# Optimization experiments

Measured on AMD Instinct MI355X. Metric: run time of the kernel, lower is better.

The kernel has to match this reference:

```python
import jax, jax.numpy as jnp
import numpy as np

D_MODEL, D_LOW, NUM_BINS = 512, 64, 39
DIST_MIN, DIST_MAX = 2.0, 22.0
BIN_WIDTH = (DIST_MAX - DIST_MIN) / (NUM_BINS - 1)
LN_EPS = 1e-5


def setup_inputs() -> dict:
    key = jax.random.key(0)
    ks = jax.random.split(key, 10)
    B, N = 2, 768
    h_res = jax.random.normal(ks[0], (B, N, D_MODEL), dtype=jnp.float32)
    # scale coords so pairwise distances span the [2, 22] bin range
    x_true = jax.random.normal(ks[1], (B, N, 3), dtype=jnp.float32) * 5.0
    token_pad_mask = jnp.ones((B, N), dtype=jnp.float32)
    s = 1.0 / np.sqrt(D_MODEL)
    return {
        "h_res": h_res,
        "x_true": x_true,
        "token_pad_mask": token_pad_mask,
        "ln_w": jnp.ones((D_MODEL,), jnp.float32),
        "ln_b": jnp.zeros((D_MODEL,), jnp.float32),
        "wu_w": jax.random.normal(ks[2], (D_LOW, D_MODEL), jnp.float32) * s,
        "wu_b": jnp.zeros((D_LOW,), jnp.float32),
        "wv_w": jax.random.normal(ks[3], (D_LOW, D_MODEL), jnp.float32) * s,
        "wv_b": jnp.zeros((D_LOW,), jnp.float32),
        "wb_w": jax.random.normal(ks[4], (NUM_BINS, D_LOW), jnp.float32) * (1.0 / np.sqrt(D_LOW)),
        "wb_b": jnp.zeros((NUM_BINS,), jnp.float32),
    }


def _layernorm(x, w, b):
    mu = jnp.mean(x, axis=-1, keepdims=True)
    var = jnp.mean(jnp.square(x - mu), axis=-1, keepdims=True)
    return (x - mu) * jax.lax.rsqrt(var + LN_EPS) * w + b


def reference(h_res, x_true, token_pad_mask, ln_w, ln_b, wu_w, wu_b, wv_w, wv_b, wb_w, wb_b):
    B, N, _ = h_res.shape
    # pairwise distances -> target bins (trunc-to-int then clamp, as torch .long())
    diff = x_true[:, :, None, :] - x_true[:, None, :, :]          # [B,N,N,3]
    d_true = jnp.sqrt(jnp.sum(diff * diff, axis=-1))               # [B,N,N]
    target = jnp.clip(((d_true - DIST_MIN) / BIN_WIDTH).astype(jnp.int32), 0, NUM_BINS - 1)

    h = _layernorm(h_res, ln_w, ln_b)
    U = h @ wu_w.T + wu_b                                          # [B,N,d_low]
    V = h @ wv_w.T + wv_b                                          # [B,N,d_low]
    # logits[b,i,j,k] = sum_c U[b,i,c] V[b,j,c] Wb[k,c] + bb[k]
    logits = jnp.einsum("bic,bjc,kc->bijk", U, V, wb_w) + wb_b     # [B,N,N,K]
    logp = jax.nn.log_softmax(logits, axis=-1)
    ce = -jnp.take_along_axis(logp, target[..., None], axis=-1)[..., 0]  # [B,N,N]

    mask = (token_pad_mask[:, :, None] * token_pad_mask[:, None, :]) > 0  # [B,N,N] bool
    counts = jnp.sum(mask, axis=(1, 2))                            # [B]
    per_sample = jnp.sum(jnp.where(mask, ce, 0.0), axis=(1, 2)) / jnp.maximum(counts, 1)
    valid = counts > 0
    total_count = jnp.sum(valid)
    loss = jnp.sum(jnp.where(valid, per_sample, 0.0)) / jnp.maximum(total_count, 1)
    return loss
```

## Files before the change

kernel.cpp:

```cpp
#include <hip/hip_runtime.h>
#include <hip/hip_bf16.h>
#include <math.h>

#define D_MODEL 512
#define D_LOW   64
#define NBINS   39
#define LOG2E   1.4426950408889634f
#define LN2     0.6931471805599453f

typedef __attribute__((ext_vector_type(8))) short short8;
typedef __attribute__((ext_vector_type(4))) float floatx4;

__global__ __launch_bounds__(256) void prep_tbin_kernel(
    const float* __restrict__ ln_w, const float* __restrict__ ln_b,
    const float* __restrict__ wu_w, const float* __restrict__ wu_b,
    const float* __restrict__ wv_w, const float* __restrict__ wv_b,
    const float* __restrict__ x_true, const float* __restrict__ pmask,
    __hip_bfloat16* __restrict__ w2bf, float* __restrict__ w2sum,
    float* __restrict__ b2, signed char* __restrict__ tbg, int N) {
  const int tid = threadIdx.x;

  if ((int)blockIdx.x >= 128) {
    const int p = blockIdx.x - 128;
    const int b = (p >= N) ? 1 : 0;
    const int i = p - b * N;
    const int rowi = b * N + i;
    const float xi0 = x_true[rowi * 3 + 0];
    const float xi1 = x_true[rowi * 3 + 1];
    const float xi2 = x_true[rowi * 3 + 2];
    const float pmi = pmask[rowi];
    const float BW  = (22.0f - 2.0f) / 38.0f;
    signed char* tbp = tbg + (size_t)b * N * N + (size_t)i * N;
    for (int j = tid; j < N; j += 256) {
      const int rowj = b * N + j;
      const float dx = xi0 - x_true[rowj * 3 + 0];
      const float dy = xi1 - x_true[rowj * 3 + 1];
      const float dz = xi2 - x_true[rowj * 3 + 2];
      const float d  = sqrtf(dx * dx + dy * dy + dz * dz);
      int tb = (int)((d - 2.0f) / BW);
      tb = tb < 0 ? 0 : (tb > NBINS - 1 ? NBINS - 1 : tb);
      tbp[j] = (pmi * pmask[rowj] > 0.f) ? (signed char)tb : (signed char)-1;
    }
    return;
  }

  __shared__ float red[8];
  const int o = blockIdx.x;
  const bool isU = (o < 64);
  const float* wrow = isU ? (wu_w + o * D_MODEL) : (wv_w + (o - 64) * D_MODEL);
  const float scale = isU ? LOG2E : 1.0f;

  float s1 = 0.f, s2 = 0.f;
  #pragma unroll
  for (int cc = 0; cc < 2; ++cc) {
    const int c = tid + cc * 256;
    const float w  = wrow[c];
    const float w2 = w * ln_w[c] * scale;
    const __hip_bfloat16 hb = __float2bfloat16(w2);
    w2bf[o * D_MODEL + c] = hb;
    s1 += __bfloat162float(hb);
    s2 += w * ln_b[c];
  }
  #pragma unroll
  for (int off = 32; off; off >>= 1) {
    s1 += __shfl_xor(s1, off);
    s2 += __shfl_xor(s2, off);
  }
  const int wave = tid >> 6, lane = tid & 63;
  if (lane == 0) { red[wave] = s1; red[4 + wave] = s2; }
  __syncthreads();
  if (tid == 0) {
    w2sum[o] = red[0] + red[1] + red[2] + red[3];
    const float ss2 = red[4] + red[5] + red[6] + red[7];
    b2[o] = scale * ((isU ? wu_b[o] : wv_b[o - 64]) + ss2);
  }
}

__global__ __launch_bounds__(64) void lnproj_kernel(
    const float* __restrict__ h_res, const __hip_bfloat16* __restrict__ w2bf,
    const float* __restrict__ w2sum, const float* __restrict__ b2,
    float* __restrict__ U, __hip_bfloat16* __restrict__ Vbf, int N) {
  const int lane = threadIdx.x;
  const int q = lane >> 4, ln16 = lane & 15;
  const int rt = blockIdx.x >> 2, og = blockIdx.x & 3;
  const int row0 = rt * 16;
  const float* hp = h_res + (size_t)(row0 + ln16) * D_MODEL + q * 8;

  short8 abf[16];
  float sum = 0.f, ssq = 0.f;
  #pragma unroll
  for (int kc = 0; kc < 16; ++kc) {
    const floatx4 x0 = *reinterpret_cast<const floatx4*>(hp + kc * 32);
    const floatx4 x1 = *reinterpret_cast<const floatx4*>(hp + kc * 32 + 4);
    short8 a;
    #pragma unroll
    for (int e = 0; e < 4; ++e) {
      sum += x0[e]; ssq += x0[e] * x0[e];
      const __hip_bfloat16 hb = __float2bfloat16(x0[e]);
      a[e] = *reinterpret_cast<const short*>(&hb);
    }
    #pragma unroll
    for (int e = 0; e < 4; ++e) {
      sum += x1[e]; ssq += x1[e] * x1[e];
      const __hip_bfloat16 hb = __float2bfloat16(x1[e]);
      a[4 + e] = *reinterpret_cast<const short*>(&hb);
    }
    abf[kc] = a;
  }
  sum += __shfl_xor(sum, 16); sum += __shfl_xor(sum, 32);
  ssq += __shfl_xor(ssq, 16); ssq += __shfl_xor(ssq, 32);
  const float mu  = sum * (1.0f / (float)D_MODEL);
  const float var = ssq * (1.0f / (float)D_MODEL) - mu * mu;
  const float rs  = rsqrtf(var + 1e-5f);
  float mu_r[4], rs_r[4];
  #pragma unroll
  for (int r = 0; r < 4; ++r) {
    mu_r[r] = __shfl(mu, q * 4 + r);
    rs_r[r] = __shfl(rs, q * 4 + r);
  }

  const int obase = og * 32;
  const int out0 = obase + ln16;
  const int out1 = obase + 16 + ln16;
  const short* wp = reinterpret_cast<const short*>(w2bf);
  floatx4 acc0 = (floatx4){0.f, 0.f, 0.f, 0.f};
  floatx4 acc1 = (floatx4){0.f, 0.f, 0.f, 0.f};
  #pragma unroll
  for (int kc = 0; kc < 16; ++kc) {
    const short8 b0 = *reinterpret_cast<const short8*>(
        wp + (size_t)out0 * D_MODEL + kc * 32 + q * 8);
    const short8 b1 = *reinterpret_cast<const short8*>(
        wp + (size_t)out1 * D_MODEL + kc * 32 + q * 8);
    acc0 = __builtin_amdgcn_mfma_f32_16x16x32_bf16(abf[kc], b0, acc0, 0, 0, 0);
    acc1 = __builtin_amdgcn_mfma_f32_16x16x32_bf16(abf[kc], b1, acc1, 0, 0, 0);
  }

  #pragma unroll
  for (int nt = 0; nt < 2; ++nt) {
    const int out  = nt ? out1 : out0;
    const floatx4 a = nt ? acc1 : acc0;
    const float ws = w2sum[out];
    const float bb = b2[out];
    #pragma unroll
    for (int r = 0; r < 4; ++r) {
      const int rowg = row0 + q * 4 + r;
      const float val = rs_r[r] * a[r] - mu_r[r] * rs_r[r] * ws + bb;
      if (out < 64) {
        U[(size_t)rowg * D_LOW + out] = val;
      } else {
        Vbf[(size_t)rowg * D_LOW + (out - 64)] = __float2bfloat16(val);
      }
    }
  }
}

__global__ __launch_bounds__(256) void wprep_kernel(
    const float* __restrict__ U, const float* __restrict__ wb_w,
    short* __restrict__ wfragbuf, int BN) {
  __shared__ float wsh[NBINS * 65];
  const int tid = threadIdx.x;
  for (int e = tid; e < NBINS * D_LOW; e += 256) {
    const int n = e >> 6, c = e & 63;
    wsh[n * 65 + c] = wb_w[e];
  }
  __syncthreads();

  const int wave = tid >> 6, lane = tid & 63;
  const int q = lane >> 4, ln16 = lane & 15;
  const int rowi = blockIdx.x * 4 + wave;
  const float* Up = U + (size_t)rowi * D_LOW;

  float u[16];
  #pragma unroll
  for (int s = 0; s < 2; ++s)
    #pragma unroll
    for (int e = 0; e < 8; ++e) u[s * 8 + e] = Up[s * 32 + q * 8 + e];

  short* outp = wfragbuf + (size_t)rowi * 6 * 64 * 8;
  #pragma unroll
  for (int t = 0; t < 3; ++t) {
    const int n = t * 16 + ln16;
    #pragma unroll
    for (int s = 0; s < 2; ++s) {
      short8 f;
      #pragma unroll
      for (int e = 0; e < 8; ++e) {
        const float w = (n < NBINS) ? wsh[n * 65 + s * 32 + q * 8 + e] : 0.f;
        const float v = u[s * 8 + e] * w;
        const __hip_bfloat16 hb = __float2bfloat16(v);
        f[e] = *reinterpret_cast<const short*>(&hb);
      }
      *reinterpret_cast<short8*>(outp + ((size_t)(t * 2 + s) * 64 + lane) * 8) = f;
    }
  }
}

__global__ __launch_bounds__(256) void pair_mfma_kernel(
    const short* __restrict__ wfragbuf,
    const __hip_bfloat16* __restrict__ Vbf,
    const float* __restrict__ wb_b,
    const signed char* __restrict__ tbg,
    float* __restrict__ part, int N) {
  __shared__ float rbuf[8];
  const int i    = blockIdx.x;
  const int b    = blockIdx.y >> 1;
  const int half = blockIdx.y & 1;
  const int tid  = threadIdx.x;
  const int wave = tid >> 6, lane = tid & 63;
  const int q = lane >> 4, ln16 = lane & 15;
  const int rowi = b * N + i;

  short8 wfrag[3][2];
  {
    const short* wfp = wfragbuf + (size_t)rowi * 6 * 64 * 8;
    #pragma unroll
    for (int t = 0; t < 3; ++t)
      #pragma unroll
      for (int s = 0; s < 2; ++s)
        wfrag[t][s] = *reinterpret_cast<const short8*>(
            wfp + ((size_t)(t * 2 + s) * 64 + lane) * 8);
  }

  floatx4 bias_init[3];
  #pragma unroll
  for (int t = 0; t < 3; ++t)
    #pragma unroll
    for (int r = 0; r < 4; ++r) {
      const int bin = t * 16 + q * 4 + r;
      bias_init[t][r] = (bin < NBINS) ? LOG2E * wb_b[bin] : -INFINITY;
    }

  const short* Vp = reinterpret_cast<const short*>(Vbf) + (size_t)b * N * D_LOW;
  const signed char* tbp = tbg + (size_t)b * N * N + (size_t)i * N;
  const int jbase = half * 384 + wave * 96;
  const int q4 = q * 4;

  float ce_sum = 0.f, cnt_sum = 0.f;

  short8 v[2][2];
  int tbv[2];
  {
    #pragma unroll
    for (int tt = 0; tt < 2; ++tt) {
      const size_t jr = jbase + tt * 16 + ln16;
      v[tt][0] = *reinterpret_cast<const short8*>(Vp + jr * D_LOW + q * 8);
      v[tt][1] = *reinterpret_cast<const short8*>(Vp + jr * D_LOW + 32 + q * 8);
      tbv[tt]  = (int)tbp[jr];
    }
  }

  for (int g = 0; g < 3; ++g) {
    short8 vn[2][2];
    int tbn[2];
    if (g < 2) {
      const int jb = jbase + (g + 1) * 32;
      #pragma unroll
      for (int tt = 0; tt < 2; ++tt) {
        const size_t jr = jb + tt * 16 + ln16;
        vn[tt][0] = *reinterpret_cast<const short8*>(Vp + jr * D_LOW + q * 8);
        vn[tt][1] = *reinterpret_cast<const short8*>(Vp + jr * D_LOW + 32 + q * 8);
        tbn[tt]   = (int)tbp[jr];
      }
    }

    floatx4 f[2][3];
    #pragma unroll
    for (int tt = 0; tt < 2; ++tt)
      #pragma unroll
      for (int t = 0; t < 3; ++t) {
        floatx4 a = bias_init[t];
        a = __builtin_amdgcn_mfma_f32_16x16x32_bf16(wfrag[t][0], v[tt][0], a, 0, 0, 0);
        a = __builtin_amdgcn_mfma_f32_16x16x32_bf16(wfrag[t][1], v[tt][1], a, 0, 0, 0);
        f[tt][t] = a;
      }

    #pragma unroll
    for (int tt = 0; tt < 2; ++tt) {
      const int tb  = tbv[tt];
      const int tbq = tb - q4;
      float s0 = 0.f, s1 = 0.f, s2 = 0.f, s3 = 0.f, lt = 0.f;
      #pragma unroll
      for (int t = 0; t < 3; ++t) {
        const floatx4 fv = f[tt][t];
        s0 += __builtin_amdgcn_exp2f(fv[0]);
        s1 += __builtin_amdgcn_exp2f(fv[1]);
        s2 += __builtin_amdgcn_exp2f(fv[2]);
        s3 += __builtin_amdgcn_exp2f(fv[3]);
        lt += (tbq == t * 16 + 0) ? fv[0] : 0.f;
        lt += (tbq == t * 16 + 1) ? fv[1] : 0.f;
        lt += (tbq == t * 16 + 2) ? fv[2] : 0.f;
        lt += (tbq == t * 16 + 3) ? fv[3] : 0.f;
      }
      float ssum = (s0 + s1) + (s2 + s3);
      ssum += __shfl_xor(ssum, 16); ssum += __shfl_xor(ssum, 32);
      const float ok = (tb >= 0) ? 1.f : 0.f;
      ce_sum  += ok * LN2 * (__builtin_amdgcn_logf(ssum) - 4.0f * lt);
      cnt_sum += ok;
    }

    if (g < 2) {
      #pragma unroll
      for (int tt = 0; tt < 2; ++tt) {
        v[tt][0] = vn[tt][0]; v[tt][1] = vn[tt][1]; tbv[tt] = tbn[tt];
      }
    }
  }

  #pragma unroll
  for (int off = 32; off; off >>= 1) {
    ce_sum  += __shfl_xor(ce_sum, off);
    cnt_sum += __shfl_xor(cnt_sum, off);
  }
  if (lane == 0) { rbuf[wave] = ce_sum; rbuf[4 + wave] = cnt_sum; }
  __syncthreads();
  if (tid == 0) {
    const size_t slot = ((size_t)(b * 2 + half) * N + i) * 2;
    part[slot + 0] = rbuf[0] + rbuf[1] + rbuf[2] + rbuf[3];
    part[slot + 1] = rbuf[4] + rbuf[5] + rbuf[6] + rbuf[7];
  }
}

__global__ __launch_bounds__(256) void finalize_kernel(
    const float* __restrict__ part, float* __restrict__ out, int N, int B) {
  __shared__ float red[8];
  const int tid = threadIdx.x, wave = tid >> 6, lane = tid & 63;
  float loss = 0.f, vcount = 0.f;
  for (int b = 0; b < B; ++b) {
    float ce = 0.f, cnt = 0.f;
    for (int e = tid; e < 2 * N; e += 256) {
      const size_t base = ((size_t)b * 2 * N + e) * 2;
      ce  += part[base + 0];
      cnt += part[base + 1];
    }
    #pragma unroll
    for (int off = 32; off; off >>= 1) {
      ce  += __shfl_xor(ce, off);
      cnt += __shfl_xor(cnt, off);
    }
    if (lane == 0) { red[wave] = ce; red[4 + wave] = cnt; }
    __syncthreads();
    if (tid == 0) {
      const float s = red[0] + red[1] + red[2] + red[3];
      const float c = red[4] + red[5] + red[6] + red[7];
      if (c > 0.f) { loss += s / fmaxf(c, 1.f); vcount += 1.f; }
    }
    __syncthreads();
  }
  if (tid == 0) out[0] = (vcount > 0.f) ? loss / vcount : 0.f;
}

extern "C" void kernel_launch(void* const* d_in, const int* in_sizes, int n_in,
                              void* d_out, int out_size, void* d_ws, size_t ws_size,
                              hipStream_t stream) {
  const float* h_res  = (const float*)d_in[0];
  const float* x_true = (const float*)d_in[1];
  const float* pmask  = (const float*)d_in[2];
  const float* ln_w   = (const float*)d_in[3];
  const float* ln_b   = (const float*)d_in[4];
  const float* wu_w   = (const float*)d_in[5];
  const float* wu_b   = (const float*)d_in[6];
  const float* wv_w   = (const float*)d_in[7];
  const float* wv_b   = (const float*)d_in[8];
  const float* wb_w   = (const float*)d_in[9];
  const float* wb_b   = (const float*)d_in[10];

  const int B  = 2;
  const int N  = in_sizes[2] / B;
  const int BN = B * N;

  float* U = (float*)d_ws;
  __hip_bfloat16* Vbf = (__hip_bfloat16*)(U + (size_t)BN * D_LOW);
  float* part = (float*)(Vbf + (size_t)BN * D_LOW);
  signed char* tbg = (signed char*)(part + 4 * (size_t)BN);
  short* wfragbuf = (short*)(tbg + (size_t)B * N * N);
  __hip_bfloat16* w2bf = (__hip_bfloat16*)(wfragbuf + (size_t)BN * 6 * 64 * 8);
  float* w2sum = (float*)(w2bf + 128 * D_MODEL);
  float* b2    = w2sum + 128;

  prep_tbin_kernel<<<128 + BN, 256, 0, stream>>>(
      ln_w, ln_b, wu_w, wu_b, wv_w, wv_b, x_true, pmask,
      w2bf, w2sum, b2, tbg, N);
  lnproj_kernel<<<(BN / 16) * 4, 64, 0, stream>>>(h_res, w2bf, w2sum, b2,
                                                  U, Vbf, N);
  wprep_kernel<<<BN / 4, 256, 0, stream>>>(U, wb_w, wfragbuf, BN);
  pair_mfma_kernel<<<dim3(N, 2 * B), 256, 0, stream>>>(wfragbuf, Vbf, wb_b,
                                                       tbg, part, N);
  finalize_kernel<<<1, 256, 0, stream>>>(part, (float*)d_out, N, B);
}
```

Before: 118.5 us.

## Fuse target-bin computation into pair kernel and merge projection with wfrag prep

```diff
diff --git a/kernel.cpp b/kernel.cpp
--- a/kernel.cpp
+++ b/kernel.cpp
@@ -11,26 +11,179 @@
 typedef __attribute__((ext_vector_type(8))) short short8;
 typedef __attribute__((ext_vector_type(4))) float floatx4;
 
-__global__ __launch_bounds__(256) void prep_tbin_kernel(
+__global__ __launch_bounds__(256) void prep_kernel(
     const float* __restrict__ ln_w, const float* __restrict__ ln_b,
     const float* __restrict__ wu_w, const float* __restrict__ wu_b,
     const float* __restrict__ wv_w, const float* __restrict__ wv_b,
+    __hip_bfloat16* __restrict__ w2bf, float* __restrict__ w2sum,
+    float* __restrict__ b2) {
+  __shared__ float red[8];
+  const int tid = threadIdx.x;
+  const int o = blockIdx.x;
+  const bool isU = (o < 64);
+  const float* wrow = isU ? (wu_w + o * D_MODEL) : (wv_w + (o - 64) * D_MODEL);
+  const float scale = isU ? LOG2E : 1.0f;
+
+  float s1 = 0.f, s2 = 0.f;
+  #pragma unroll
+  for (int cc = 0; cc < 2; ++cc) {
+    const int c = tid + cc * 256;
+    const float w  = wrow[c];
+    const float w2 = w * ln_w[c] * scale;
+    const __hip_bfloat16 hb = __float2bfloat16(w2);
+    w2bf[o * D_MODEL + c] = hb;
+    s1 += __bfloat162float(hb);
+    s2 += w * ln_b[c];
+  }
+  #pragma unroll
+  for (int off = 32; off; off >>= 1) {
+    s1 += __shfl_xor(s1, off);
+    s2 += __shfl_xor(s2, off);
+  }
+  const int wave = tid >> 6, lane = tid & 63;
+  if (lane == 0) { red[wave] = s1; red[4 + wave] = s2; }
+  __syncthreads();
+  if (tid == 0) {
+    w2sum[o] = red[0] + red[1] + red[2] + red[3];
+    const float ss2 = red[4] + red[5] + red[6] + red[7];
+    b2[o] = scale * ((isU ? wu_b[o] : wv_b[o - 64]) + ss2);
+  }
+}
+
+__global__ __launch_bounds__(256) void lnproj_wprep_kernel(
+    const float* __restrict__ h_res, const __hip_bfloat16* __restrict__ w2bf,
+    const float* __restrict__ w2sum, const float* __restrict__ b2,
+    const float* __restrict__ wb_w,
+    __hip_bfloat16* __restrict__ Vbf, short* __restrict__ wfragbuf, int N) {
+  __shared__ float Urow[16][D_LOW];
+  __shared__ float wsh[NBINS * 65];
+  const int tid  = threadIdx.x;
+  const int wave = tid >> 6, lane = tid & 63;
+  const int q = lane >> 4, ln16 = lane & 15;
+  const int row0 = blockIdx.x * 16;
+
+  for (int e = tid; e < NBINS * D_LOW; e += 256) {
+    wsh[(e >> 6) * 65 + (e & 63)] = wb_w[e];
+  }
+
+  const float* hp = h_res + (size_t)(row0 + ln16) * D_MODEL + q * 8;
+  short8 abf[16];
+  float sum = 0.f, ssq = 0.f;
+  #pragma unroll
+  for (int kc = 0; kc < 16; ++kc) {
+    const floatx4 x0 = *reinterpret_cast<const floatx4*>(hp + kc * 32);
+    const floatx4 x1 = *reinterpret_cast<const floatx4*>(hp + kc * 32 + 4);
+    short8 a;
+    #pragma unroll
+    for (int e = 0; e < 4; ++e) {
+      sum += x0[e]; ssq += x0[e] * x0[e];
+      const __hip_bfloat16 hb = __float2bfloat16(x0[e]);
+      a[e] = *reinterpret_cast<const short*>(&hb);
+    }
+    #pragma unroll
+    for (int e = 0; e < 4; ++e) {
+      sum += x1[e]; ssq += x1[e] * x1[e];
+      const __hip_bfloat16 hb = __float2bfloat16(x1[e]);
+      a[4 + e] = *reinterpret_cast<const short*>(&hb);
+    }
+    abf[kc] = a;
+  }
+  sum += __shfl_xor(sum, 16); sum += __shfl_xor(sum, 32);
+  ssq += __shfl_xor(ssq, 16); ssq += __shfl_xor(ssq, 32);
+  const float mu  = sum * (1.0f / (float)D_MODEL);
+  const float var = ssq * (1.0f / (float)D_MODEL) - mu * mu;
+  const float rs  = rsqrtf(var + 1e-5f);
+  float mu_r[4], rs_r[4];
+  #pragma unroll
+  for (int r = 0; r < 4; ++r) {
+    mu_r[r] = __shfl(mu, q * 4 + r);
+    rs_r[r] = __shfl(rs, q * 4 + r);
+  }
+
+  const int obase = wave * 32;
+  const int out0 = obase + ln16;
+  const int out1 = obase + 16 + ln16;
+  const short* wp = reinterpret_cast<const short*>(w2bf);
+  floatx4 acc0 = (floatx4){0.f, 0.f, 0.f, 0.f};
+  floatx4 acc1 = (floatx4){0.f, 0.f, 0.f, 0.f};
+  #pragma unroll
+  for (int kc = 0; kc < 16; ++kc) {
+    const short8 b0 = *reinterpret_cast<const short8*>(
+        wp + (size_t)out0 * D_MODEL + kc * 32 + q * 8);
+    const short8 b1 = *reinterpret_cast<const short8*>(
+        wp + (size_t)out1 * D_MODEL + kc * 32 + q * 8);
+    acc0 = __builtin_amdgcn_mfma_f32_16x16x32_bf16(abf[kc], b0, acc0, 0, 0, 0);
+    acc1 = __builtin_amdgcn_mfma_f32_16x16x32_bf16(abf[kc], b1, acc1, 0, 0, 0);
+  }
+
+  #pragma unroll
+  for (int nt = 0; nt < 2; ++nt) {
+    const int out  = nt ? out1 : out0;
+    const floatx4 a = nt ? acc1 : acc0;
+    const float ws = w2sum[out];
+    const float bb = b2[out];
+    #pragma unroll
+    for (int r = 0; r < 4; ++r) {
+      const int rloc = q * 4 + r;
+      const float val = rs_r[r] * a[r] - mu_r[r] * rs_r[r] * ws + bb;
+      if (out < 64) {
+        Urow[rloc][out] = val;
+      } else {
+        Vbf[(size_t)(row0 + rloc) * D_LOW + (out - 64)] = __float2bfloat16(val);
+      }
+    }
+  }
+  __syncthreads();
+
+  #pragma unroll
+  for (int rr = 0; rr < 4; ++rr) {
+    const int rloc = wave * 4 + rr;
+    const int rowi = row0 + rloc;
+    float u[16];
+    #pragma unroll
+    for (int s = 0; s < 2; ++s)
+      #pragma unroll
+      for (int e = 0; e < 8; ++e) u[s * 8 + e] = Urow[rloc][s * 32 + q * 8 + e];
+    short* outp = wfragbuf + (size_t)rowi * 6 * 64 * 8;
+    #pragma unroll
+    for (int t = 0; t < 3; ++t) {
+      const int n = t * 16 + ln16;
+      #pragma unroll
+      for (int s = 0; s < 2; ++s) {
+        short8 f;
+        #pragma unroll
+        for (int e = 0; e < 8; ++e) {
+          const float w = (n < NBINS) ? wsh[n * 65 + s * 32 + q * 8 + e] : 0.f;
+          const float v = u[s * 8 + e] * w;
+          const __hip_bfloat16 hb = __float2bfloat16(v);
+          f[e] = *reinterpret_cast<const short*>(&hb);
+        }
+        *reinterpret_cast<short8*>(outp + ((size_t)(t * 2 + s) * 64 + lane) * 8) = f;
+      }
+    }
+  }
+}
+
+__global__ __launch_bounds__(256) void pair_mfma_kernel(
+    const short* __restrict__ wfragbuf,
+    const __hip_bfloat16* __restrict__ Vbf,
     const float* __restrict__ x_true, const float* __restrict__ pmask,
-    __hip_bfloat16* __restrict__ w2bf, float* __restrict__ w2sum,
-    float* __restrict__ b2, signed char* __restrict__ tbg, int N) {
-  const int tid = threadIdx.x;
-
-  if ((int)blockIdx.x >= 128) {
-    const int p = blockIdx.x - 128;
-    const int b = (p >= N) ? 1 : 0;
-    const int i = p - b * N;
-    const int rowi = b * N + i;
+    const float* __restrict__ wb_b,
+    float* __restrict__ part, int N) {
+  __shared__ int tbm[768];
+  __shared__ float rbuf[8];
+  const int i = blockIdx.x, b = blockIdx.y;
+  const int tid  = threadIdx.x;
+  const int wave = tid >> 6, lane = tid & 63;
+  const int q = lane >> 4, ln16 = lane & 15;
+  const int rowi = b * N + i;
+
+  {
     const float xi0 = x_true[rowi * 3 + 0];
     const float xi1 = x_true[rowi * 3 + 1];
     const float xi2 = x_true[rowi * 3 + 2];
     const float pmi = pmask[rowi];
     const float BW  = (22.0f - 2.0f) / 38.0f;
-    signed char* tbp = tbg + (size_t)b * N * N + (size_t)i * N;
     for (int j = tid; j < N; j += 256) {
       const int rowj = b * N + j;
       const float dx = xi0 - x_true[rowj * 3 + 0];
@@ -39,176 +192,9 @@
       const float d  = sqrtf(dx * dx + dy * dy + dz * dz);
       int tb = (int)((d - 2.0f) / BW);
       tb = tb < 0 ? 0 : (tb > NBINS - 1 ? NBINS - 1 : tb);
-      tbp[j] = (pmi * pmask[rowj] > 0.f) ? (signed char)tb : (signed char)-1;
-    }
-    return;
-  }
-
-  __shared__ float red[8];
-  const int o = blockIdx.x;
-  const bool isU = (o < 64);
-  const float* wrow = isU ? (wu_w + o * D_MODEL) : (wv_w + (o - 64) * D_MODEL);
-  const float scale = isU ? LOG2E : 1.0f;
-
-  float s1 = 0.f, s2 = 0.f;
-  #pragma unroll
-  for (int cc = 0; cc < 2; ++cc) {
-    const int c = tid + cc * 256;
-    const float w  = wrow[c];
-    const float w2 = w * ln_w[c] * scale;
-    const __hip_bfloat16 hb = __float2bfloat16(w2);
-    w2bf[o * D_MODEL + c] = hb;
-    s1 += __bfloat162float(hb);
-    s2 += w * ln_b[c];
-  }
-  #pragma unroll
-  for (int off = 32; off; off >>= 1) {
-    s1 += __shfl_xor(s1, off);
-    s2 += __shfl_xor(s2, off);
-  }
-  const int wave = tid >> 6, lane = tid & 63;
-  if (lane == 0) { red[wave] = s1; red[4 + wave] = s2; }
-  __syncthreads();
-  if (tid == 0) {
-    w2sum[o] = red[0] + red[1] + red[2] + red[3];
-    const float ss2 = red[4] + red[5] + red[6] + red[7];
-    b2[o] = scale * ((isU ? wu_b[o] : wv_b[o - 64]) + ss2);
-  }
-}
-
-__global__ __launch_bounds__(64) void lnproj_kernel(
-    const float* __restrict__ h_res, const __hip_bfloat16* __restrict__ w2bf,
-    const float* __restrict__ w2sum, const float* __restrict__ b2,
-    float* __restrict__ U, __hip_bfloat16* __restrict__ Vbf, int N) {
-  const int lane = threadIdx.x;
-  const int q = lane >> 4, ln16 = lane & 15;
-  const int rt = blockIdx.x >> 2, og = blockIdx.x & 3;
-  const int row0 = rt * 16;
-  const float* hp = h_res + (size_t)(row0 + ln16) * D_MODEL + q * 8;
-
-  short8 abf[16];
-  float sum = 0.f, ssq = 0.f;
-  #pragma unroll
-  for (int kc = 0; kc < 16; ++kc) {
-    const floatx4 x0 = *reinterpret_cast<const floatx4*>(hp + kc * 32);
-    const floatx4 x1 = *reinterpret_cast<const floatx4*>(hp + kc * 32 + 4);
-    short8 a;
-    #pragma unroll
-    for (int e = 0; e < 4; ++e) {
-      sum += x0[e]; ssq += x0[e] * x0[e];
-      const __hip_bfloat16 hb = __float2bfloat16(x0[e]);
-      a[e] = *reinterpret_cast<const short*>(&hb);
-    }
-    #pragma unroll
-    for (int e = 0; e < 4; ++e) {
-      sum += x1[e]; ssq += x1[e] * x1[e];
-      const __hip_bfloat16 hb = __float2bfloat16(x1[e]);
-      a[4 + e] = *reinterpret_cast<const short*>(&hb);
-    }
-    abf[kc] = a;
-  }
-  sum += __shfl_xor(sum, 16); sum += __shfl_xor(sum, 32);
-  ssq += __shfl_xor(ssq, 16); ssq += __shfl_xor(ssq, 32);
-  const float mu  = sum * (1.0f / (float)D_MODEL);
-  const float var = ssq * (1.0f / (float)D_MODEL) - mu * mu;
-  const float rs  = rsqrtf(var + 1e-5f);
-  float mu_r[4], rs_r[4];
-  #pragma unroll
-  for (int r = 0; r < 4; ++r) {
-    mu_r[r] = __shfl(mu, q * 4 + r);
-    rs_r[r] = __shfl(rs, q * 4 + r);
-  }
-
-  const int obase = og * 32;
-  const int out0 = obase + ln16;
-  const int out1 = obase + 16 + ln16;
-  const short* wp = reinterpret_cast<const short*>(w2bf);
-  floatx4 acc0 = (floatx4){0.f, 0.f, 0.f, 0.f};
-  floatx4 acc1 = (floatx4){0.f, 0.f, 0.f, 0.f};
-  #pragma unroll
-  for (int kc = 0; kc < 16; ++kc) {
-    const short8 b0 = *reinterpret_cast<const short8*>(
-        wp + (size_t)out0 * D_MODEL + kc * 32 + q * 8);
-    const short8 b1 = *reinterpret_cast<const short8*>(
-        wp + (size_t)out1 * D_MODEL + kc * 32 + q * 8);
-    acc0 = __builtin_amdgcn_mfma_f32_16x16x32_bf16(abf[kc], b0, acc0, 0, 0, 0);
-    acc1 = __builtin_amdgcn_mfma_f32_16x16x32_bf16(abf[kc], b1, acc1, 0, 0, 0);
-  }
-
-  #pragma unroll
-  for (int nt = 0; nt < 2; ++nt) {
-    const int out  = nt ? out1 : out0;
-    const floatx4 a = nt ? acc1 : acc0;
-    const float ws = w2sum[out];
-    const float bb = b2[out];
-    #pragma unroll
-    for (int r = 0; r < 4; ++r) {
-      const int rowg = row0 + q * 4 + r;
-      const float val = rs_r[r] * a[r] - mu_r[r] * rs_r[r] * ws + bb;
-      if (out < 64) {
-        U[(size_t)rowg * D_LOW + out] = val;
-      } else {
-        Vbf[(size_t)rowg * D_LOW + (out - 64)] = __float2bfloat16(val);
-      }
-    }
-  }
-}
-
-__global__ __launch_bounds__(256) void wprep_kernel(
-    const float* __restrict__ U, const float* __restrict__ wb_w,
-    short* __restrict__ wfragbuf, int BN) {
-  __shared__ float wsh[NBINS * 65];
-  const int tid = threadIdx.x;
-  for (int e = tid; e < NBINS * D_LOW; e += 256) {
-    const int n = e >> 6, c = e & 63;
-    wsh[n * 65 + c] = wb_w[e];
-  }
-  __syncthreads();
-
-  const int wave = tid >> 6, lane = tid & 63;
-  const int q = lane >> 4, ln16 = lane & 15;
-  const int rowi = blockIdx.x * 4 + wave;
-  const float* Up = U + (size_t)rowi * D_LOW;
-
-  float u[16];
-  #pragma unroll
-  for (int s = 0; s < 2; ++s)
-    #pragma unroll
-    for (int e = 0; e < 8; ++e) u[s * 8 + e] = Up[s * 32 + q * 8 + e];
-
-  short* outp = wfragbuf + (size_t)rowi * 6 * 64 * 8;
-  #pragma unroll
-  for (int t = 0; t < 3; ++t) {
-    const int n = t * 16 + ln16;
-    #pragma unroll
-    for (int s = 0; s < 2; ++s) {
-      short8 f;
-      #pragma unroll
-      for (int e = 0; e < 8; ++e) {
-        const float w = (n < NBINS) ? wsh[n * 65 + s * 32 + q * 8 + e] : 0.f;
-        const float v = u[s * 8 + e] * w;
-        const __hip_bfloat16 hb = __float2bfloat16(v);
-        f[e] = *reinterpret_cast<const short*>(&hb);
-      }
-      *reinterpret_cast<short8*>(outp + ((size_t)(t * 2 + s) * 64 + lane) * 8) = f;
-    }
-  }
-}
-
-__global__ __launch_bounds__(256) void pair_mfma_kernel(
-    const short* __restrict__ wfragbuf,
-    const __hip_bfloat16* __restrict__ Vbf,
-    const float* __restrict__ wb_b,
-    const signed char* __restrict__ tbg,
-    float* __restrict__ part, int N) {
-  __shared__ float rbuf[8];
-  const int i    = blockIdx.x;
-  const int b    = blockIdx.y >> 1;
-  const int half = blockIdx.y & 1;
-  const int tid  = threadIdx.x;
-  const int wave = tid >> 6, lane = tid & 63;
-  const int q = lane >> 4, ln16 = lane & 15;
-  const int rowi = b * N + i;
+      tbm[j] = (pmi * pmask[rowj] > 0.f) ? tb : -1;
+    }
+  }
 
   short8 wfrag[3][2];
   {
@@ -230,36 +216,35 @@
       bias_init[t][r] = (bin < NBINS) ? LOG2E * wb_b[bin] : -INFINITY;
     }
 
+  __syncthreads();
+
   const short* Vp = reinterpret_cast<const short*>(Vbf) + (size_t)b * N * D_LOW;
-  const signed char* tbp = tbg + (size_t)b * N * N + (size_t)i * N;
-  const int jbase = half * 384 + wave * 96;
+  const int jbase = wave * 192;
   const int q4 = q * 4;
 
   float ce_sum = 0.f, cnt_sum = 0.f;
 
   short8 v[2][2];
   int tbv[2];
-  {
-    #pragma unroll
-    for (int tt = 0; tt < 2; ++tt) {
-      const size_t jr = jbase + tt * 16 + ln16;
-      v[tt][0] = *reinterpret_cast<const short8*>(Vp + jr * D_LOW + q * 8);
-      v[tt][1] = *reinterpret_cast<const short8*>(Vp + jr * D_LOW + 32 + q * 8);
-      tbv[tt]  = (int)tbp[jr];
-    }
-  }
-
-  for (int g = 0; g < 3; ++g) {
+  #pragma unroll
+  for (int tt = 0; tt < 2; ++tt) {
+    const size_t jr = jbase + tt * 16 + ln16;
+    v[tt][0] = *reinterpret_cast<const short8*>(Vp + jr * D_LOW + q * 8);
+    v[tt][1] = *reinterpret_cast<const short8*>(Vp + jr * D_LOW + 32 + q * 8);
+    tbv[tt]  = tbm[jr];
+  }
+
+  for (int g = 0; g < 6; ++g) {
     short8 vn[2][2];
     int tbn[2];
-    if (g < 2) {
+    if (g < 5) {
       const int jb = jbase + (g + 1) * 32;
       #pragma unroll
       for (int tt = 0; tt < 2; ++tt) {
         const size_t jr = jb + tt * 16 + ln16;
         vn[tt][0] = *reinterpret_cast<const short8*>(Vp + jr * D_LOW + q * 8);
         vn[tt][1] = *reinterpret_cast<const short8*>(Vp + jr * D_LOW + 32 + q * 8);
-        tbn[tt]   = (int)tbp[jr];
+        tbn[tt]   = tbm[jr];
       }
     }
 
@@ -298,7 +283,7 @@
       cnt_sum += ok;
     }
 
-    if (g < 2) {
+    if (g < 5) {
       #pragma unroll
       for (int tt = 0; tt < 2; ++tt) {
         v[tt][0] = vn[tt][0]; v[tt][1] = vn[tt][1]; tbv[tt] = tbn[tt];
@@ -314,9 +299,8 @@
   if (lane == 0) { rbuf[wave] = ce_sum; rbuf[4 + wave] = cnt_sum; }
   __syncthreads();
   if (tid == 0) {
-    const size_t slot = ((size_t)(b * 2 + half) * N + i) * 2;
-    part[slot + 0] = rbuf[0] + rbuf[1] + rbuf[2] + rbuf[3];
-    part[slot + 1] = rbuf[4] + rbuf[5] + rbuf[6] + rbuf[7];
+    part[rowi * 2 + 0] = rbuf[0] + rbuf[1] + rbuf[2] + rbuf[3];
+    part[rowi * 2 + 1] = rbuf[4] + rbuf[5] + rbuf[6] + rbuf[7];
   }
 }
 
@@ -327,10 +311,9 @@
   float loss = 0.f, vcount = 0.f;
   for (int b = 0; b < B; ++b) {
     float ce = 0.f, cnt = 0.f;
-    for (int e = tid; e < 2 * N; e += 256) {
-      const size_t base = ((size_t)b * 2 * N + e) * 2;
-      ce  += part[base + 0];
-      cnt += part[base + 1];
+    for (int i = tid; i < N; i += 256) {
+      ce  += part[(b * N + i) * 2 + 0];
+      cnt += part[(b * N + i) * 2 + 1];
     }
     #pragma unroll
     for (int off = 32; off; off >>= 1) {
@@ -368,22 +351,18 @@
   const int N  = in_sizes[2] / B;
   const int BN = B * N;
 
-  float* U = (float*)d_ws;
-  __hip_bfloat16* Vbf = (__hip_bfloat16*)(U + (size_t)BN * D_LOW);
+  __hip_bfloat16* Vbf = (__hip_bfloat16*)d_ws;
   float* part = (float*)(Vbf + (size_t)BN * D_LOW);
-  signed char* tbg = (signed char*)(part + 4 * (size_t)BN);
-  short* wfragbuf = (short*)(tbg + (size_t)B * N * N);
+  short* wfragbuf = (short*)(part + 2 * (size_t)BN);
   __hip_bfloat16* w2bf = (__hip_bfloat16*)(wfragbuf + (size_t)BN * 6 * 64 * 8);
   float* w2sum = (float*)(w2bf + 128 * D_MODEL);
   float* b2    = w2sum + 128;
 
-  prep_tbin_kernel<<<128 + BN, 256, 0, stream>>>(
-      ln_w, ln_b, wu_w, wu_b, wv_w, wv_b, x_true, pmask,
-      w2bf, w2sum, b2, tbg, N);
-  lnproj_kernel<<<(BN / 16) * 4, 64, 0, stream>>>(h_res, w2bf, w2sum, b2,
-                                                  U, Vbf, N);
-  wprep_kernel<<<BN / 4, 256, 0, stream>>>(U, wb_w, wfragbuf, BN);
-  pair_mfma_kernel<<<dim3(N, 2 * B), 256, 0, stream>>>(wfragbuf, Vbf, wb_b,
-                                                       tbg, part, N);
+  prep_kernel<<<128, 256, 0, stream>>>(ln_w, ln_b, wu_w, wu_b, wv_w, wv_b,
+                                       w2bf, w2sum, b2);
+  lnproj_wprep_kernel<<<BN / 16, 256, 0, stream>>>(h_res, w2bf, w2sum, b2,
+                                                   wb_w, Vbf, wfragbuf, N);
+  pair_mfma_kernel<<<dim3(N, B), 256, 0, stream>>>(wfragbuf, Vbf, x_true,
+                                                   pmask, wb_b, part, N);
   finalize_kernel<<<1, 256, 0, stream>>>(part, (float*)d_out, N, B);
 }
```

Measured after the change: 123.2 us. +4.0%, slower.

## Fuse all stages into one cooperative persistent kernel with grid syncs

Applied to the files above, without the earlier changes.

```diff
diff --git a/kernel.cpp b/kernel.cpp
--- a/kernel.cpp
+++ b/kernel.cpp
@@ -1,6 +1,9 @@
 #include <hip/hip_runtime.h>
 #include <hip/hip_bf16.h>
+#include <hip/hip_cooperative_groups.h>
 #include <math.h>
+
+namespace cg = cooperative_groups;
 
 #define D_MODEL 512
 #define D_LOW   64
@@ -11,7 +14,323 @@
 typedef __attribute__((ext_vector_type(8))) short short8;
 typedef __attribute__((ext_vector_type(4))) float floatx4;
 
-__global__ __launch_bounds__(256) void prep_tbin_kernel(
+__global__ __launch_bounds__(256, 2) void mega_kernel(
+    const float* __restrict__ h_res,
+    const float* __restrict__ x_true,
+    const float* __restrict__ pmask,
+    const float* __restrict__ ln_w, const float* __restrict__ ln_b,
+    const float* __restrict__ wu_w, const float* __restrict__ wu_b,
+    const float* __restrict__ wv_w, const float* __restrict__ wv_b,
+    const float* __restrict__ wb_w, const float* __restrict__ wb_b,
+    __hip_bfloat16* __restrict__ Vbf,
+    signed char* __restrict__ tbg,
+    short* __restrict__ wfragbuf,
+    __hip_bfloat16* __restrict__ w2bf,
+    float* __restrict__ w2sum, float* __restrict__ b2,
+    float* __restrict__ part,
+    float* __restrict__ out,
+    int N) {
+  cg::grid_group grid = cg::this_grid();
+  __shared__ float Urow[16][D_LOW];
+  __shared__ float wsh[NBINS * 65];
+  __shared__ float red[32];
+  const int nb  = gridDim.x;
+  const int bid = blockIdx.x;
+  const int tid = threadIdx.x;
+  const int wave = tid >> 6, lane = tid & 63;
+  const int q = lane >> 4, ln16 = lane & 15;
+  const int B  = 2;
+  const int BN = B * N;
+
+  if (bid < 128) {
+    const int o = bid;
+    const bool isU = (o < 64);
+    const float* wrow = isU ? (wu_w + o * D_MODEL) : (wv_w + (o - 64) * D_MODEL);
+    const float scale = isU ? LOG2E : 1.0f;
+    float s1 = 0.f, s2 = 0.f;
+    #pragma unroll
+    for (int cc = 0; cc < 2; ++cc) {
+      const int c = tid + cc * 256;
+      const float w  = wrow[c];
+      const float w2 = w * ln_w[c] * scale;
+      const __hip_bfloat16 hb = __float2bfloat16(w2);
+      w2bf[o * D_MODEL + c] = hb;
+      s1 += __bfloat162float(hb);
+      s2 += w * ln_b[c];
+    }
+    #pragma unroll
+    for (int off = 32; off; off >>= 1) {
+      s1 += __shfl_xor(s1, off);
+      s2 += __shfl_xor(s2, off);
+    }
+    if (lane == 0) { red[wave] = s1; red[4 + wave] = s2; }
+    __syncthreads();
+    if (tid == 0) {
+      w2sum[o] = red[0] + red[1] + red[2] + red[3];
+      const float ss2 = red[4] + red[5] + red[6] + red[7];
+      b2[o] = scale * ((isU ? wu_b[o] : wv_b[o - 64]) + ss2);
+    }
+  }
+  for (int row = bid; row < BN; row += nb) {
+    const int b = (row >= N) ? 1 : 0;
+    const int i = row - b * N;
+    const float xi0 = x_true[row * 3 + 0];
+    const float xi1 = x_true[row * 3 + 1];
+    const float xi2 = x_true[row * 3 + 2];
+    const float pmi = pmask[row];
+    const float BW  = (22.0f - 2.0f) / 38.0f;
+    signed char* tbp = tbg + (size_t)b * N * N + (size_t)i * N;
+    for (int j = tid; j < N; j += 256) {
+      const int rowj = b * N + j;
+      const float dx = xi0 - x_true[rowj * 3 + 0];
+      const float dy = xi1 - x_true[rowj * 3 + 1];
+      const float dz = xi2 - x_true[rowj * 3 + 2];
+      const float d  = sqrtf(dx * dx + dy * dy + dz * dz);
+      int tb = (int)((d - 2.0f) / BW);
+      tb = tb < 0 ? 0 : (tb > NBINS - 1 ? NBINS - 1 : tb);
+      tbp[j] = (pmi * pmask[rowj] > 0.f) ? (signed char)tb : (signed char)-1;
+    }
+  }
+  __threadfence();
+  grid.sync();
+
+  if (bid < BN / 16) {
+    for (int e = tid; e < NBINS * D_LOW; e += 256) {
+      wsh[(e >> 6) * 65 + (e & 63)] = wb_w[e];
+    }
+    const int row0 = bid * 16;
+    const float* hp = h_res + (size_t)(row0 + ln16) * D_MODEL + q * 8;
+    short8 abf[16];
+    float sum = 0.f, ssq = 0.f;
+    #pragma unroll
+    for (int kc = 0; kc < 16; ++kc) {
+      const floatx4 x0 = *reinterpret_cast<const floatx4*>(hp + kc * 32);
+      const floatx4 x1 = *reinterpret_cast<const floatx4*>(hp + kc * 32 + 4);
+      short8 a;
+      #pragma unroll
+      for (int e = 0; e < 4; ++e) {
+        sum += x0[e]; ssq += x0[e] * x0[e];
+        const __hip_bfloat16 hb = __float2bfloat16(x0[e]);
+        a[e] = *reinterpret_cast<const short*>(&hb);
+      }
+      #pragma unroll
+      for (int e = 0; e < 4; ++e) {
+        sum += x1[e]; ssq += x1[e] * x1[e];
+        const __hip_bfloat16 hb = __float2bfloat16(x1[e]);
+        a[4 + e] = *reinterpret_cast<const short*>(&hb);
+      }
+      abf[kc] = a;
+    }
+    sum += __shfl_xor(sum, 16); sum += __shfl_xor(sum, 32);
+    ssq += __shfl_xor(ssq, 16); ssq += __shfl_xor(ssq, 32);
+    const float mu  = sum * (1.0f / (float)D_MODEL);
+    const float var = ssq * (1.0f / (float)D_MODEL) - mu * mu;
+    const float rs  = rsqrtf(var + 1e-5f);
+    float mu_r[4], rs_r[4];
+    #pragma unroll
+    for (int r = 0; r < 4; ++r) {
+      mu_r[r] = __shfl(mu, q * 4 + r);
+      rs_r[r] = __shfl(rs, q * 4 + r);
+    }
+
+    const int obase = wave * 32;
+    const int out0 = obase + ln16;
+    const int out1 = obase + 16 + ln16;
+    const short* wp = reinterpret_cast<const short*>(w2bf);
+    floatx4 acc0 = (floatx4){0.f, 0.f, 0.f, 0.f};
+    floatx4 acc1 = (floatx4){0.f, 0.f, 0.f, 0.f};
+    #pragma unroll
+    for (int kc = 0; kc < 16; ++kc) {
+      const short8 b0 = *reinterpret_cast<const short8*>(
+          wp + (size_t)out0 * D_MODEL + kc * 32 + q * 8);
+      const short8 b1 = *reinterpret_cast<const short8*>(
+          wp + (size_t)out1 * D_MODEL + kc * 32 + q * 8);
+      acc0 = __builtin_amdgcn_mfma_f32_16x16x32_bf16(abf[kc], b0, acc0, 0, 0, 0);
+      acc1 = __builtin_amdgcn_mfma_f32_16x16x32_bf16(abf[kc], b1, acc1, 0, 0, 0);
+    }
+
+    #pragma unroll
+    for (int nt = 0; nt < 2; ++nt) {
+      const int out_ = nt ? out1 : out0;
+      const floatx4 a = nt ? acc1 : acc0;
+      const float ws = w2sum[out_];
+      const float bb = b2[out_];
+      #pragma unroll
+      for (int r = 0; r < 4; ++r) {
+        const int rloc = q * 4 + r;
+        const float val = rs_r[r] * a[r] - mu_r[r] * rs_r[r] * ws + bb;
+        if (out_ < 64) {
+          Urow[rloc][out_] = val;
+        } else {
+          Vbf[(size_t)(row0 + rloc) * D_LOW + (out_ - 64)] = __float2bfloat16(val);
+        }
+      }
+    }
+    __syncthreads();
+
+    #pragma unroll
+    for (int rr = 0; rr < 4; ++rr) {
+      const int rloc = wave * 4 + rr;
+      const int rowi = row0 + rloc;
+      float u[16];
+      #pragma unroll
+      for (int s = 0; s < 2; ++s)
+        #pragma unroll
+        for (int e = 0; e < 8; ++e) u[s * 8 + e] = Urow[rloc][s * 32 + q * 8 + e];
+      short* outp = wfragbuf + (size_t)rowi * 6 * 64 * 8;
+      #pragma unroll
+      for (int t = 0; t < 3; ++t) {
+        const int n = t * 16 + ln16;
+        #pragma unroll
+        for (int s = 0; s < 2; ++s) {
+          short8 f;
+          #pragma unroll
+          for (int e = 0; e < 8; ++e) {
+            const float w = (n < NBINS) ? wsh[n * 65 + s * 32 + q * 8 + e] : 0.f;
+            const float v = u[s * 8 + e] * w;
+            const __hip_bfloat16 hb = __float2bfloat16(v);
+            f[e] = *reinterpret_cast<const short*>(&hb);
+          }
+          *reinterpret_cast<short8*>(outp + ((size_t)(t * 2 + s) * 64 + lane) * 8) = f;
+        }
+      }
+    }
+  }
+  __threadfence();
+  grid.sync();
+
+  floatx4 bias_init[3];
+  #pragma unroll
+  for (int t = 0; t < 3; ++t)
+    #pragma unroll
+    for (int r = 0; r < 4; ++r) {
+      const int bin = t * 16 + q * 4 + r;
+      bias_init[t][r] = (bin < NBINS) ? LOG2E * wb_b[bin] : -INFINITY;
+    }
+  const int q4 = q * 4;
+  float ce_acc[2]  = {0.f, 0.f};
+  float cnt_acc[2] = {0.f, 0.f};
+
+  for (int k = 0; k < 6; ++k) {
+    const int u = bid + k * nb;
+    if (u >= 4 * N) break;
+    const int i    = u >> 2;
+    const int b    = (u >> 1) & 1;
+    const int half = u & 1;
+    const int rowi = b * N + i;
+
+    short8 wfrag[3][2];
+    {
+      const short* wfp = wfragbuf + (size_t)rowi * 6 * 64 * 8;
+      #pragma unroll
+      for (int t = 0; t < 3; ++t)
+        #pragma unroll
+        for (int s = 0; s < 2; ++s)
+          wfrag[t][s] = *reinterpret_cast<const short8*>(
+              wfp + ((size_t)(t * 2 + s) * 64 + lane) * 8);
+    }
+    const short* Vp = reinterpret_cast<const short*>(Vbf) + (size_t)b * N * D_LOW;
+    const signed char* tbp = tbg + (size_t)b * N * N + (size_t)i * N;
+    const int jbase = half * 384 + wave * 96;
+
+    float ce_u = 0.f, cnt_u = 0.f;
+    for (int g = 0; g < 3; ++g) {
+      const int jb = jbase + g * 32;
+      short8 v[2][2];
+      int tbv[2];
+      #pragma unroll
+      for (int tt = 0; tt < 2; ++tt) {
+        const size_t jr = jb + tt * 16 + ln16;
+        v[tt][0] = *reinterpret_cast<const short8*>(Vp + jr * D_LOW + q * 8);
+        v[tt][1] = *reinterpret_cast<const short8*>(Vp + jr * D_LOW + 32 + q * 8);
+        tbv[tt]  = (int)tbp[jr];
+      }
+
+      #pragma unroll
+      for (int tt = 0; tt < 2; ++tt) {
+        floatx4 f[3];
+        #pragma unroll
+        for (int t = 0; t < 3; ++t) {
+          floatx4 a = bias_init[t];
+          a = __builtin_amdgcn_mfma_f32_16x16x32_bf16(wfrag[t][0], v[tt][0], a, 0, 0, 0);
+          a = __builtin_amdgcn_mfma_f32_16x16x32_bf16(wfrag[t][1], v[tt][1], a, 0, 0, 0);
+          f[t] = a;
+        }
+        const int tb  = tbv[tt];
+        const int tbq = tb - q4;
+        float s0 = 0.f, s1 = 0.f, s2 = 0.f, s3 = 0.f, lt = 0.f;
+        #pragma unroll
+        for (int t = 0; t < 3; ++t) {
+          const floatx4 fv = f[t];
+          s0 += __builtin_amdgcn_exp2f(fv[0]);
+          s1 += __builtin_amdgcn_exp2f(fv[1]);
+          s2 += __builtin_amdgcn_exp2f(fv[2]);
+          s3 += __builtin_amdgcn_exp2f(fv[3]);
+          lt += (tbq == t * 16 + 0) ? fv[0] : 0.f;
+          lt += (tbq == t * 16 + 1) ? fv[1] : 0.f;
+          lt += (tbq == t * 16 + 2) ? fv[2] : 0.f;
+          lt += (tbq == t * 16 + 3) ? fv[3] : 0.f;
+        }
+        float ssum = (s0 + s1) + (s2 + s3);
+        ssum += __shfl_xor(ssum, 16); ssum += __shfl_xor(ssum, 32);
+        const float ok = (tb >= 0) ? 1.f : 0.f;
+        ce_u  += ok * LN2 * (__builtin_amdgcn_logf(ssum) - 4.0f * lt);
+        cnt_u += ok;
+      }
+    }
+    ce_acc[0]  += (b == 0) ? ce_u : 0.f;
+    ce_acc[1]  += (b == 1) ? ce_u : 0.f;
+    cnt_acc[0] += (b == 0) ? cnt_u : 0.f;
+    cnt_acc[1] += (b == 1) ? cnt_u : 0.f;
+  }
+
+  #pragma unroll
+  for (int off = 32; off; off >>= 1) {
+    ce_acc[0]  += __shfl_xor(ce_acc[0], off);
+    ce_acc[1]  += __shfl_xor(ce_acc[1], off);
+    cnt_acc[0] += __shfl_xor(cnt_acc[0], off);
+    cnt_acc[1] += __shfl_xor(cnt_acc[1], off);
+  }
+  if (lane == 0) {
+    float* ps = part + ((size_t)bid * 4 + wave) * 4;
+    ps[0] = ce_acc[0]; ps[1] = cnt_acc[0];
+    ps[2] = ce_acc[1]; ps[3] = cnt_acc[1];
+  }
+  __threadfence();
+  grid.sync();
+
+  if (bid == 0) {
+    float ce0 = 0.f, cn0 = 0.f, ce1 = 0.f, cn1 = 0.f;
+    for (int e = tid; e < nb * 4; e += 256) {
+      const float* ps = part + (size_t)e * 4;
+      ce0 += ps[0]; cn0 += ps[1]; ce1 += ps[2]; cn1 += ps[3];
+    }
+    #pragma unroll
+    for (int off = 32; off; off >>= 1) {
+      ce0 += __shfl_xor(ce0, off); cn0 += __shfl_xor(cn0, off);
+      ce1 += __shfl_xor(ce1, off); cn1 += __shfl_xor(cn1, off);
+    }
+    if (lane == 0) {
+      red[wave * 4 + 0] = ce0; red[wave * 4 + 1] = cn0;
+      red[wave * 4 + 2] = ce1; red[wave * 4 + 3] = cn1;
+    }
+    __syncthreads();
+    if (tid == 0) {
+      float tce0 = 0.f, tcn0 = 0.f, tce1 = 0.f, tcn1 = 0.f;
+      #pragma unroll
+      for (int w = 0; w < 4; ++w) {
+        tce0 += red[w * 4 + 0]; tcn0 += red[w * 4 + 1];
+        tce1 += red[w * 4 + 2]; tcn1 += red[w * 4 + 3];
+      }
+      float loss = 0.f, vc = 0.f;
+      if (tcn0 > 0.f) { loss += tce0 / fmaxf(tcn0, 1.f); vc += 1.f; }
+      if (tcn1 > 0.f) { loss += tce1 / fmaxf(tcn1, 1.f); vc += 1.f; }
+      out[0] = (vc > 0.f) ? loss / vc : 0.f;
+    }
+  }
+}
+
+__global__ __launch_bounds__(256) void fb_prep_tbin_kernel(
     const float* __restrict__ ln_w, const float* __restrict__ ln_b,
     const float* __restrict__ wu_w, const float* __restrict__ wu_b,
     const float* __restrict__ wv_w, const float* __restrict__ wv_b,
@@ -19,7 +338,6 @@
     __hip_bfloat16* __restrict__ w2bf, float* __restrict__ w2sum,
     float* __restrict__ b2, signed char* __restrict__ tbg, int N) {
   const int tid = threadIdx.x;
-
   if ((int)blockIdx.x >= 128) {
     const int p = blockIdx.x - 128;
     const int b = (p >= N) ? 1 : 0;
@@ -43,13 +361,11 @@
     }
     return;
   }
-
   __shared__ float red[8];
   const int o = blockIdx.x;
   const bool isU = (o < 64);
   const float* wrow = isU ? (wu_w + o * D_MODEL) : (wv_w + (o - 64) * D_MODEL);
   const float scale = isU ? LOG2E : 1.0f;
-
   float s1 = 0.f, s2 = 0.f;
   #pragma unroll
   for (int cc = 0; cc < 2; ++cc) {
@@ -76,7 +392,7 @@
   }
 }
 
-__global__ __launch_bounds__(64) void lnproj_kernel(
+__global__ __launch_bounds__(64) void fb_lnproj_kernel(
     const float* __restrict__ h_res, const __hip_bfloat16* __restrict__ w2bf,
     const float* __restrict__ w2sum, const float* __restrict__ b2,
     float* __restrict__ U, __hip_bfloat16* __restrict__ Vbf, int N) {
@@ -85,7 +401,6 @@
   const int rt = blockIdx.x >> 2, og = blockIdx.x & 3;
   const int row0 = rt * 16;
   const float* hp = h_res + (size_t)(row0 + ln16) * D_MODEL + q * 8;
-
   short8 abf[16];
   float sum = 0.f, ssq = 0.f;
   #pragma unroll
@@ -118,7 +433,6 @@
     mu_r[r] = __shfl(mu, q * 4 + r);
     rs_r[r] = __shfl(rs, q * 4 + r);
   }
-
   const int obase = og * 32;
   const int out0 = obase + ln16;
   const int out1 = obase + 16 + ln16;
@@ -134,10 +448,9 @@
     acc0 = __builtin_amdgcn_mfma_f32_16x16x32_bf16(abf[kc], b0, acc0, 0, 0, 0);
     acc1 = __builtin_amdgcn_mfma_f32_16x16x32_bf16(abf[kc], b1, acc1, 0, 0, 0);
   }
-
   #pragma unroll
   for (int nt = 0; nt < 2; ++nt) {
-    const int out  = nt ? out1 : out0;
+    const int out = nt ? out1 : out0;
     const floatx4 a = nt ? acc1 : acc0;
     const float ws = w2sum[out];
     const float bb = b2[out];
@@ -154,28 +467,24 @@
   }
 }
 
-__global__ __launch_bounds__(256) void wprep_kernel(
+__global__ __launch_bounds__(256) void fb_wprep_kernel(
     const float* __restrict__ U, const float* __restrict__ wb_w,
     short* __restrict__ wfragbuf, int BN) {
   __shared__ float wsh[NBINS * 65];
   const int tid = threadIdx.x;
   for (int e = tid; e < NBINS * D_LOW; e += 256) {
-    const int n = e >> 6, c = e & 63;
-    wsh[n * 65 + c] = wb_w[e];
+    wsh[(e >> 6) * 65 + (e & 63)] = wb_w[e];
   }
   __syncthreads();
-
   const int wave = tid >> 6, lane = tid & 63;
   const int q = lane >> 4, ln16 = lane & 15;
   const int rowi = blockIdx.x * 4 + wave;
   const float* Up = U + (size_t)rowi * D_LOW;
-
   float u[16];
   #pragma unroll
   for (int s = 0; s < 2; ++s)
     #pragma unroll
     for (int e = 0; e < 8; ++e) u[s * 8 + e] = Up[s * 32 + q * 8 + e];
-
   short* outp = wfragbuf + (size_t)rowi * 6 * 64 * 8;
   #pragma unroll
   for (int t = 0; t < 3; ++t) {
@@ -195,7 +504,7 @@
   }
 }
 
-__global__ __launch_bounds__(256) void pair_mfma_kernel(
+__global__ __launch_bounds__(256) void fb_pair_mfma_kernel(
     const short* __restrict__ wfragbuf,
     const __hip_bfloat16* __restrict__ Vbf,
     const float* __restrict__ wb_b,
@@ -209,7 +518,6 @@
   const int wave = tid >> 6, lane = tid & 63;
   const int q = lane >> 4, ln16 = lane & 15;
   const int rowi = b * N + i;
-
   short8 wfrag[3][2];
   {
     const short* wfp = wfragbuf + (size_t)rowi * 6 * 64 * 8;
@@ -220,7 +528,6 @@
         wfrag[t][s] = *reinterpret_cast<const short8*>(
             wfp + ((size_t)(t * 2 + s) * 64 + lane) * 8);
   }
-
   floatx4 bias_init[3];
   #pragma unroll
   for (int t = 0; t < 3; ++t)
@@ -229,59 +536,38 @@
       const int bin = t * 16 + q * 4 + r;
       bias_init[t][r] = (bin < NBINS) ? LOG2E * wb_b[bin] : -INFINITY;
     }
-
   const short* Vp = reinterpret_cast<const short*>(Vbf) + (size_t)b * N * D_LOW;
   const signed char* tbp = tbg + (size_t)b * N * N + (size_t)i * N;
   const int jbase = half * 384 + wave * 96;
   const int q4 = q * 4;
-
   float ce_sum = 0.f, cnt_sum = 0.f;
-
-  short8 v[2][2];
-  int tbv[2];
-  {
+  for (int g = 0; g < 3; ++g) {
+    const int jb = jbase + g * 32;
+    short8 v[2][2];
+    int tbv[2];
     #pragma unroll
     for (int tt = 0; tt < 2; ++tt) {
-      const size_t jr = jbase + tt * 16 + ln16;
+      const size_t jr = jb + tt * 16 + ln16;
       v[tt][0] = *reinterpret_cast<const short8*>(Vp + jr * D_LOW + q * 8);
       v[tt][1] = *reinterpret_cast<const short8*>(Vp + jr * D_LOW + 32 + q * 8);
       tbv[tt]  = (int)tbp[jr];
     }
-  }
-
-  for (int g = 0; g < 3; ++g) {
-    short8 vn[2][2];
-    int tbn[2];
-    if (g < 2) {
-      const int jb = jbase + (g + 1) * 32;
-      #pragma unroll
-      for (int tt = 0; tt < 2; ++tt) {
-        const size_t jr = jb + tt * 16 + ln16;
-        vn[tt][0] = *reinterpret_cast<const short8*>(Vp + jr * D_LOW + q * 8);
-        vn[tt][1] = *reinterpret_cast<const short8*>(Vp + jr * D_LOW + 32 + q * 8);
-        tbn[tt]   = (int)tbp[jr];
-      }
-    }
-
-    floatx4 f[2][3];
-    #pragma unroll
-    for (int tt = 0; tt < 2; ++tt)
+    #pragma unroll
+    for (int tt = 0; tt < 2; ++tt) {
+      floatx4 f[3];
       #pragma unroll
       for (int t = 0; t < 3; ++t) {
         floatx4 a = bias_init[t];
         a = __builtin_amdgcn_mfma_f32_16x16x32_bf16(wfrag[t][0], v[tt][0], a, 0, 0, 0);
         a = __builtin_amdgcn_mfma_f32_16x16x32_bf16(wfrag[t][1], v[tt][1], a, 0, 0, 0);
-        f[tt][t] = a;
-      }
-
-    #pragma unroll
-    for (int tt = 0; tt < 2; ++tt) {
+        f[t] = a;
+      }
       const int tb  = tbv[tt];
       const int tbq = tb - q4;
       float s0 = 0.f, s1 = 0.f, s2 = 0.f, s3 = 0.f, lt = 0.f;
       #pragma unroll
       for (int t = 0; t < 3; ++t) {
-        const floatx4 fv = f[tt][t];
+        const floatx4 fv = f[t];
         s0 += __builtin_amdgcn_exp2f(fv[0]);
         s1 += __builtin_amdgcn_exp2f(fv[1]);
         s2 += __builtin_amdgcn_exp2f(fv[2]);
@@ -297,15 +583,7 @@
       ce_sum  += ok * LN2 * (__builtin_amdgcn_logf(ssum) - 4.0f * lt);
       cnt_sum += ok;
     }
-
-    if (g < 2) {
-      #pragma unroll
-      for (int tt = 0; tt < 2; ++tt) {
-        v[tt][0] = vn[tt][0]; v[tt][1] = vn[tt][1]; tbv[tt] = tbn[tt];
-      }
-    }
-  }
-
+  }
   #pragma unroll
   for (int off = 32; off; off >>= 1) {
     ce_sum  += __shfl_xor(ce_sum, off);
@@ -320,7 +598,7 @@
   }
 }
 
-__global__ __launch_bounds__(256) void finalize_kernel(
+__global__ __launch_bounds__(256) void fb_finalize_kernel(
     const float* __restrict__ part, float* __restrict__ out, int N, int B) {
   __shared__ float red[8];
   const int tid = threadIdx.x, wave = tid >> 6, lane = tid & 63;
@@ -365,25 +643,38 @@
   const float* wb_b   = (const float*)d_in[10];
 
   const int B  = 2;
-  const int N  = in_sizes[2] / B;
+  int N  = in_sizes[2] / B;
   const int BN = B * N;
 
-  float* U = (float*)d_ws;
-  __hip_bfloat16* Vbf = (__hip_bfloat16*)(U + (size_t)BN * D_LOW);
-  float* part = (float*)(Vbf + (size_t)BN * D_LOW);
-  signed char* tbg = (signed char*)(part + 4 * (size_t)BN);
+  __hip_bfloat16* Vbf = (__hip_bfloat16*)d_ws;
+  float* U = (float*)(Vbf + (size_t)BN * D_LOW);
+  float* part = U + (size_t)BN * D_LOW;
+  signed char* tbg = (signed char*)(part + 16 * (size_t)BN);
   short* wfragbuf = (short*)(tbg + (size_t)B * N * N);
   __hip_bfloat16* w2bf = (__hip_bfloat16*)(wfragbuf + (size_t)BN * 6 * 64 * 8);
   float* w2sum = (float*)(w2bf + 128 * D_MODEL);
   float* b2    = w2sum + 128;
-
-  prep_tbin_kernel<<<128 + BN, 256, 0, stream>>>(
-      ln_w, ln_b, wu_w, wu_b, wv_w, wv_b, x_true, pmask,
-      w2bf, w2sum, b2, tbg, N);
-  lnproj_kernel<<<(BN / 16) * 4, 64, 0, stream>>>(h_res, w2bf, w2sum, b2,
-                                                  U, Vbf, N);
-  wprep_kernel<<<BN / 4, 256, 0, stream>>>(U, wb_w, wfragbuf, BN);
-  pair_mfma_kernel<<<dim3(N, 2 * B), 256, 0, stream>>>(wfragbuf, Vbf, wb_b,
-                                                       tbg, part, N);
-  finalize_kernel<<<1, 256, 0, stream>>>(part, (float*)d_out, N, B);
+  float* outp  = (float*)d_out;
+
+  void* args[] = {
+    (void*)&h_res, (void*)&x_true, (void*)&pmask,
+    (void*)&ln_w, (void*)&ln_b, (void*)&wu_w, (void*)&wu_b,
+    (void*)&wv_w, (void*)&wv_b, (void*)&wb_w, (void*)&wb_b,
+    (void*)&Vbf, (void*)&tbg, (void*)&wfragbuf, (void*)&w2bf,
+    (void*)&w2sum, (void*)&b2, (void*)&part, (void*)&outp, (void*)&N
+  };
+  hipError_t err = hipLaunchCooperativeKernel(
+      mega_kernel, dim3(512), dim3(256), args, 0, stream);
+
+  if (err != hipSuccess) {
+    fb_prep_tbin_kernel<<<128 + BN, 256, 0, stream>>>(
+        ln_w, ln_b, wu_w, wu_b, wv_w, wv_b, x_true, pmask,
+        w2bf, w2sum, b2, tbg, N);
+    fb_lnproj_kernel<<<(BN / 16) * 4, 64, 0, stream>>>(h_res, w2bf, w2sum, b2,
+                                                       U, Vbf, N);
+    fb_wprep_kernel<<<BN / 4, 256, 0, stream>>>(U, wb_w, wfragbuf, BN);
+    fb_pair_mfma_kernel<<<dim3(N, 2 * B), 256, 0, stream>>>(wfragbuf, Vbf,
+                                                            wb_b, tbg, part, N);
+    fb_finalize_kernel<<<1, 256, 0, stream>>>(part, (float*)d_out, N, B);
+  }
 }
```

New measurement: 421.7 us. +255.8%, slower.
